# Kernel tuning notes

Hardware: AMD Instinct MI355X
Metric: run time of the kernel (lower is better)

## Reference

```python
import jax, jax.numpy as jnp
import numpy as np

N = 50000      # nodes
E = 800000     # edges (avg degree 16)
D = 64         # node feature dim
DE = 32        # edge feature dim
H = 256        # MLP hidden dim


def setup_inputs() -> dict:
    key = jax.random.key(0)
    k0, k1, k2, k3, k4 = jax.random.split(key, 5)
    x = jax.random.normal(k0, (N, D), dtype=jnp.float32)
    edge_index = jax.random.randint(k1, (2, E), 0, N)
    edge_attr = jax.random.normal(k2, (E, DE), dtype=jnp.float32)
    fan_in1 = 2 * D + DE  # 160
    W1 = jax.random.normal(k3, (fan_in1, H), dtype=jnp.float32) / np.float32(np.sqrt(fan_in1))
    b1 = jnp.zeros((H,), dtype=jnp.float32)
    W2 = jax.random.normal(k4, (H, D), dtype=jnp.float32) / np.float32(np.sqrt(H))
    b2 = jnp.zeros((D,), dtype=jnp.float32)
    return {"x": x, "edge_index": edge_index, "edge_attr": edge_attr,
            "W1": W1, "b1": b1, "W2": W2, "b2": b2}


def reference(x, edge_index, edge_attr, W1, b1, W2, b2):
    row, col = edge_index[0], edge_index[1]
    # gather endpoint features + edge features -> [E, 2D+DE]
    feats = jnp.concatenate([x[row], x[col], edge_attr], axis=-1)
    # MLP: Linear -> ReLU -> Linear
    h = jax.nn.relu(feats @ W1 + b1)          # [E, H]
    out = h @ W2 + b2                          # [E, D]
    # scatter-max aggregate by source node (row), dim_size = N
    agg = jax.ops.segment_max(out, row, num_segments=N)  # [N, D]
    # PyG's old scatter_('max') zero-fills empty slots
    agg = jnp.where(jnp.isneginf(agg), jnp.float32(0.0), agg)
    return (agg, out)
```

## Files before the change

kernel.cpp:

```cpp
#include <hip/hip_runtime.h>
#include <hip/hip_bf16.h>
#include <math.h>

#define NNODES 50000
#define NEDGES 800000
#define CHUNKS (NEDGES / 64)
#define NBLK 256
#define GWAVES (NBLK * 8)

using short8 = __attribute__((ext_vector_type(8))) short;
using f32x4  = __attribute__((ext_vector_type(4))) float;
using f32x16 = __attribute__((ext_vector_type(16))) float;
using u32x4  = __attribute__((ext_vector_type(4))) unsigned;

__device__ __forceinline__ short f2b(float v) {
    return __builtin_bit_cast(short, __float2bfloat16(v));
}
__device__ __forceinline__ unsigned cvt2(float a, float b) {
    return (unsigned)(unsigned short)f2b(a) | ((unsigned)(unsigned short)f2b(b) << 16);
}
__device__ __forceinline__ float b2f_lo(unsigned u) {
    return __builtin_bit_cast(float, u << 16);
}
__device__ __forceinline__ float b2f_hi(unsigned u) {
    return __builtin_bit_cast(float, u & 0xFFFF0000u);
}

__global__ void prep_all(const float* __restrict__ x, short* __restrict__ xb,
                         const float* __restrict__ W1, const float* __restrict__ W2,
                         short* __restrict__ wpk, const int* __restrict__ ei,
                         unsigned* __restrict__ cnt)
{
    int b = blockIdx.x;
    if (b < 3125) {
        int i = b * 256 + threadIdx.x;
        float4 v = reinterpret_cast<const float4*>(x)[i];
        short4 o;
        o.x = f2b(v.x); o.y = f2b(v.y); o.z = f2b(v.z); o.w = f2b(v.w);
        reinterpret_cast<short4*>(xb)[i] = o;
    } else if (b < 6250) {
        int e = (b - 3125) * 256 + threadIdx.x;
        atomicAdd(&cnt[ei[e]], 1u);
    } else {
        int i = (b - 6250) * 256 + threadIdx.x;
        if (i < 40960) {
            int k = i >> 8, n = i & 255;
            int lane = (n & 31) + (((k >> 3) & 1) << 5);
            wpk[(((n >> 5) * 10 + (k >> 4)) * 64 + lane) * 8 + (k & 7)] = f2b(W1[i]);
        }
        if (i < 16384) {
            int k = i >> 6, n = i & 63;
            int lane = (n & 31) + (((k >> 3) & 1) << 5);
            wpk[40960 + (((n >> 5) * 16 + (k >> 4)) * 64 + lane) * 8 + (k & 7)] = f2b(W2[i]);
        }
    }
}

__global__ __launch_bounds__(1024)
void csr_scan1(const unsigned* __restrict__ cnt, unsigned* __restrict__ offs,
               unsigned* __restrict__ bsum) {
    __shared__ unsigned sbuf[1024];
    int t = threadIdx.x, i = blockIdx.x * 1024 + t;
    unsigned v = (i < NNODES) ? cnt[i] : 0u;
    sbuf[t] = v;
    __syncthreads();
    for (int off = 1; off < 1024; off <<= 1) {
        unsigned add = (t >= off) ? sbuf[t - off] : 0u;
        __syncthreads();
        sbuf[t] += add;
        __syncthreads();
    }
    if (i < NNODES) offs[i] = sbuf[t];
    if (t == 1023) bsum[blockIdx.x] = sbuf[1023];
}

__global__ void csr_scan2(unsigned* __restrict__ bsum) {
    int t = threadIdx.x;
    unsigned v = (t < 49) ? bsum[t] : 0u;
    unsigned orig = v;
    for (int off = 1; off < 64; off <<= 1) {
        unsigned n = __shfl_up(v, off, 64);
        if (t >= off) v += n;
    }
    if (t < 49) bsum[t] = v - orig;
}

__global__ __launch_bounds__(1024)
void csr_scan3(const unsigned* __restrict__ cnt, unsigned* __restrict__ offs,
               const unsigned* __restrict__ bsum) {
    int i = blockIdx.x * 1024 + threadIdx.x;
    if (i < NNODES)       offs[i] = offs[i] - cnt[i] + bsum[blockIdx.x];
    else if (i == NNODES) offs[i] = NEDGES;
}

__global__ void csr_place(const int* __restrict__ ei, const unsigned* __restrict__ offs,
                          unsigned* __restrict__ cur, unsigned* __restrict__ elist) {
    int e = blockIdx.x * 256 + threadIdx.x;
    if (e < NEDGES) {
        int r = ei[e];
        unsigned p = offs[r] + atomicAdd(&cur[r], 1u);
        elist[p] = (unsigned)e;
    }
}

template<bool STOREB16>
__global__ __launch_bounds__(512, 2)
void edgeconv_main(const short* __restrict__ xb, const int* __restrict__ ei,
                   const float* __restrict__ ea, const short* __restrict__ wpk,
                   const float* __restrict__ b1, const float* __restrict__ b2,
                   float* __restrict__ outbuf, unsigned* __restrict__ ob16)
{
    __shared__ short    wlds[57344];
    __shared__ unsigned tb[8][1280];

    for (int i = threadIdx.x; i < 7168; i += 512)
        reinterpret_cast<short8*>(wlds)[i] = reinterpret_cast<const short8*>(wpk)[i];
    __syncthreads();

    const short* w1s = wlds;
    const short* w2s = wlds + 40960;
    const int lane = threadIdx.x & 63;
    const int wave = threadIdx.x >> 6;
    const int l32 = lane & 31, hi = lane >> 5;
    unsigned* tw = tb[wave];
    const int gw = blockIdx.x * 8 + wave;

    int r0 = 0, r1 = 0, c0 = 0, c1 = 0;
    {
        int ea0 = gw * 64 + l32, ea1 = gw * 64 + 32 + l32;
        r0 = ei[ea0]; c0 = ei[NEDGES + ea0];
        r1 = ei[ea1]; c1 = ei[NEDGES + ea1];
    }

    for (int c = gw; c < CHUNKS; c += GWAVES) {
        int cn = c + GWAVES;
        int r0n = 0, r1n = 0, c0n = 0, c1n = 0;
        if (cn < CHUNKS) {
            int ea0 = cn * 64 + l32, ea1 = cn * 64 + 32 + l32;
            r0n = ei[ea0]; c0n = ei[NEDGES + ea0];
            r1n = ei[ea1]; c1n = ei[NEDGES + ea1];
        }

        short8 fx[2][10];
        #pragma unroll
        for (int g = 0; g < 2; ++g) {
            const int rr = g ? r1 : r0, cg = g ? c1 : c0;
            const int e = c * 64 + g * 32 + l32;
            #pragma unroll
            for (int ks = 0; ks < 4; ++ks)
                fx[g][ks] = *reinterpret_cast<const short8*>(xb + rr * 64 + ks * 16 + hi * 8);
            #pragma unroll
            for (int ks = 0; ks < 4; ++ks)
                fx[g][4 + ks] = *reinterpret_cast<const short8*>(xb + cg * 64 + ks * 16 + hi * 8);
            #pragma unroll
            for (int ks = 0; ks < 2; ++ks) {
                const float4* p = reinterpret_cast<const float4*>(ea + (size_t)e * 32 + ks * 16 + hi * 8);
                float4 a = p[0], b = p[1];
                u32x4 uu;
                uu[0] = cvt2(a.x, a.y); uu[1] = cvt2(a.z, a.w);
                uu[2] = cvt2(b.x, b.y); uu[3] = cvt2(b.z, b.w);
                fx[g][8 + ks] = __builtin_bit_cast(short8, uu);
            }
        }

        f32x16 acc2[2][2];
        #pragma unroll
        for (int t2 = 0; t2 < 2; ++t2)
            #pragma unroll
            for (int gg = 0; gg < 4; ++gg) {
                float4 bb = *reinterpret_cast<const float4*>(b2 + t2 * 32 + gg * 8 + hi * 4);
                #pragma unroll
                for (int g = 0; g < 2; ++g) {
                    acc2[t2][g][gg * 4 + 0] = bb.x; acc2[t2][g][gg * 4 + 1] = bb.y;
                    acc2[t2][g][gg * 4 + 2] = bb.z; acc2[t2][g][gg * 4 + 3] = bb.w;
                }
            }

        #pragma unroll 1
        for (int t = 0; t < 8; ++t) {
            f32x16 acc1[2];
            #pragma unroll
            for (int gg = 0; gg < 4; ++gg) {
                float4 bb = *reinterpret_cast<const float4*>(b1 + t * 32 + gg * 8 + hi * 4);
                #pragma unroll
                for (int g = 0; g < 2; ++g) {
                    acc1[g][gg * 4 + 0] = bb.x; acc1[g][gg * 4 + 1] = bb.y;
                    acc1[g][gg * 4 + 2] = bb.z; acc1[g][gg * 4 + 3] = bb.w;
                }
            }
            #pragma unroll
            for (int ks = 0; ks < 10; ++ks) {
                short8 wf = *reinterpret_cast<const short8*>(
                    w1s + ((t * 10 + ks) * 64 + lane) * 8);
                acc1[0] = __builtin_amdgcn_mfma_f32_32x32x16_bf16(wf, fx[0][ks], acc1[0], 0, 0, 0);
                acc1[1] = __builtin_amdgcn_mfma_f32_32x32x16_bf16(wf, fx[1][ks], acc1[1], 0, 0, 0);
            }
            #pragma unroll
            for (int ksl = 0; ksl < 2; ++ksl) {
                int ks2 = t * 2 + ksl;
                short8 w20 = *reinterpret_cast<const short8*>(w2s + (ks2 * 64 + lane) * 8);
                short8 w21 = *reinterpret_cast<const short8*>(w2s + ((16 + ks2) * 64 + lane) * 8);
                #pragma unroll
                for (int g = 0; g < 2; ++g) {
                    int q0 = ksl * 8;
                    unsigned D0 = cvt2(fmaxf(acc1[g][q0 + 0], 0.f), fmaxf(acc1[g][q0 + 1], 0.f));
                    unsigned D1 = cvt2(fmaxf(acc1[g][q0 + 2], 0.f), fmaxf(acc1[g][q0 + 3], 0.f));
                    unsigned D2 = cvt2(fmaxf(acc1[g][q0 + 4], 0.f), fmaxf(acc1[g][q0 + 5], 0.f));
                    unsigned D3 = cvt2(fmaxf(acc1[g][q0 + 6], 0.f), fmaxf(acc1[g][q0 + 7], 0.f));
                    asm("v_permlane32_swap_b32 %0, %1" : "+v"(D0), "+v"(D2));
                    asm("v_permlane32_swap_b32 %0, %1" : "+v"(D1), "+v"(D3));
                    u32x4 bu; bu[0] = D0; bu[1] = D1; bu[2] = D2; bu[3] = D3;
                    short8 hb = __builtin_bit_cast(short8, bu);
                    acc2[0][g] = __builtin_amdgcn_mfma_f32_32x32x16_bf16(w20, hb, acc2[0][g], 0, 0, 0);
                    acc2[1][g] = __builtin_amdgcn_mfma_f32_32x32x16_bf16(w21, hb, acc2[1][g], 0, 0, 0);
                }
            }
        }

        #pragma unroll
        for (int g = 0; g < 2; ++g) {
            const int e = c * 64 + g * 32 + l32;
            #pragma unroll
            for (int t2 = 0; t2 < 2; ++t2)
                #pragma unroll
                for (int gg = 0; gg < 4; ++gg) {
                    f32x4 v;
                    v[0] = acc2[t2][g][gg * 4 + 0]; v[1] = acc2[t2][g][gg * 4 + 1];
                    v[2] = acc2[t2][g][gg * 4 + 2]; v[3] = acc2[t2][g][gg * 4 + 3];
                    *reinterpret_cast<f32x4*>(outbuf + (size_t)e * 64 + t2 * 32 + gg * 8 + hi * 4) = v;
                }
            if (STOREB16) {
                #pragma unroll
                for (int t2 = 0; t2 < 2; ++t2)
                    #pragma unroll
                    for (int gg = 0; gg < 4; ++gg) {
                        uint2 w;
                        w.x = cvt2(acc2[t2][g][gg * 4 + 0], acc2[t2][g][gg * 4 + 1]);
                        w.y = cvt2(acc2[t2][g][gg * 4 + 2], acc2[t2][g][gg * 4 + 3]);
                        *reinterpret_cast<uint2*>(&tw[l32 * 40 + t2 * 16 + gg * 4 + hi * 2]) = w;
                    }
                asm volatile("s_waitcnt lgkmcnt(0)" ::: "memory");
                #pragma unroll
                for (int i = 0; i < 4; ++i) {
                    int row = i * 8 + (lane >> 3);
                    u32x4 v = *reinterpret_cast<const u32x4*>(&tw[row * 40 + (lane & 7) * 4]);
                    *reinterpret_cast<u32x4*>(
                        ob16 + ((size_t)(c * 64 + g * 32) * 32) + i * 256 + lane * 4) = v;
                }
                asm volatile("" ::: "memory");
            }
        }

        r0 = r0n; r1 = r1n; c0 = c0n; c1 = c1n;
    }
}

__global__ __launch_bounds__(256)
void agg_b16(const unsigned* __restrict__ offs, const unsigned* __restrict__ elist,
             const unsigned* __restrict__ ob16, float* __restrict__ agg)
{
    const int wave = threadIdx.x >> 6, lane = threadIdx.x & 63;
    const int l16 = lane & 15, qw = lane >> 4;
    const int node = blockIdx.x * 4 + wave;
    if (node >= NNODES) return;
    const unsigned s = offs[node], eend = offs[node + 1];
    float m0 = -INFINITY, m1 = -INFINITY, m2 = -INFINITY, m3 = -INFINITY;
    for (unsigned p = s + qw; p < eend; p += 4) {
        unsigned e = elist[p];
        uint2 u = *reinterpret_cast<const uint2*>(ob16 + (size_t)e * 32 + l16 * 2);
        m0 = fmaxf(m0, b2f_lo(u.x)); m1 = fmaxf(m1, b2f_hi(u.x));
        m2 = fmaxf(m2, b2f_lo(u.y)); m3 = fmaxf(m3, b2f_hi(u.y));
    }
    m0 = fmaxf(m0, __shfl_xor(m0, 16, 64)); m1 = fmaxf(m1, __shfl_xor(m1, 16, 64));
    m2 = fmaxf(m2, __shfl_xor(m2, 16, 64)); m3 = fmaxf(m3, __shfl_xor(m3, 16, 64));
    m0 = fmaxf(m0, __shfl_xor(m0, 32, 64)); m1 = fmaxf(m1, __shfl_xor(m1, 32, 64));
    m2 = fmaxf(m2, __shfl_xor(m2, 32, 64)); m3 = fmaxf(m3, __shfl_xor(m3, 32, 64));
    if (qw == 0) {
        f32x4 o;
        bool emp = (s == eend);
        o[0] = emp ? 0.0f : m0; o[1] = emp ? 0.0f : m1;
        o[2] = emp ? 0.0f : m2; o[3] = emp ? 0.0f : m3;
        *reinterpret_cast<f32x4*>(agg + (size_t)node * 64 + l16 * 4) = o;
    }
}

__global__ __launch_bounds__(256)
void agg_list(const unsigned* __restrict__ offs, const unsigned* __restrict__ elist,
              const float* __restrict__ outbuf, float* __restrict__ agg)
{
    const int wave = threadIdx.x >> 6, lane = threadIdx.x & 63;
    const int node = blockIdx.x * 4 + wave;
    if (node >= NNODES) return;
    const unsigned s = offs[node], eend = offs[node + 1];
    float m0 = -INFINITY, m1 = -INFINITY, m2 = -INFINITY, m3 = -INFINITY;
    float m4 = -INFINITY, m5 = -INFINITY, m6 = -INFINITY, m7 = -INFINITY;
    unsigned p = s;
    for (; p + 8 <= eend; p += 8) {
        float a = outbuf[(size_t)elist[p + 0] * 64 + lane];
        float b = outbuf[(size_t)elist[p + 1] * 64 + lane];
        float c = outbuf[(size_t)elist[p + 2] * 64 + lane];
        float d = outbuf[(size_t)elist[p + 3] * 64 + lane];
        float e = outbuf[(size_t)elist[p + 4] * 64 + lane];
        float f = outbuf[(size_t)elist[p + 5] * 64 + lane];
        float g = outbuf[(size_t)elist[p + 6] * 64 + lane];
        float h = outbuf[(size_t)elist[p + 7] * 64 + lane];
        m0 = fmaxf(m0, a); m1 = fmaxf(m1, b); m2 = fmaxf(m2, c); m3 = fmaxf(m3, d);
        m4 = fmaxf(m4, e); m5 = fmaxf(m5, f); m6 = fmaxf(m6, g); m7 = fmaxf(m7, h);
    }
    for (; p < eend; ++p) m0 = fmaxf(m0, outbuf[(size_t)elist[p] * 64 + lane]);
    float m = fmaxf(fmaxf(fmaxf(m0, m1), fmaxf(m2, m3)),
                    fmaxf(fmaxf(m4, m5), fmaxf(m6, m7)));
    agg[(size_t)node * 64 + lane] = (s == eend) ? 0.0f : m;
}

extern "C" void kernel_launch(void* const* d_in, const int* in_sizes, int n_in,
                              void* d_out, int out_size, void* d_ws, size_t ws_size,
                              hipStream_t stream)
{
    const float* x  = (const float*)d_in[0];
    const int*   ei = (const int*)d_in[1];
    const float* ea = (const float*)d_in[2];
    const float* W1 = (const float*)d_in[3];
    const float* b1 = (const float*)d_in[4];
    const float* W2 = (const float*)d_in[5];
    const float* b2 = (const float*)d_in[6];

    float* aggp = (float*)d_out;
    float* outp = aggp + (size_t)NNODES * 64;

    short*    xb   = (short*)d_ws;
    short*    wpk  = (short*)((char*)d_ws + 6400000);
    unsigned* meta = (unsigned*)((char*)d_ws + 6514688);
    unsigned* cnt   = meta;
    unsigned* cur   = meta + 50000;
    unsigned* offs  = meta + 100000;
    unsigned* bsum  = meta + 150016;
    unsigned* elist = meta + 150144;
    unsigned* ob16  = meta + 950144;

    const size_t NEED = 6514688ULL + 950144ULL * 4ULL + 102400000ULL;
    const bool big = ws_size >= NEED;

    (void)hipMemsetAsync(cnt, 0, 100000 * sizeof(unsigned), stream);
    prep_all<<<6410, 256, 0, stream>>>(x, xb, W1, W2, wpk, ei, cnt);
    csr_scan1<<<49, 1024, 0, stream>>>(cnt, offs, bsum);
    csr_scan2<<<1, 64, 0, stream>>>(bsum);
    csr_scan3<<<49, 1024, 0, stream>>>(cnt, offs, bsum);
    csr_place<<<NEDGES / 256, 256, 0, stream>>>(ei, offs, cur, elist);
    if (big) {
        edgeconv_main<true><<<NBLK, 512, 0, stream>>>(xb, ei, ea, wpk, b1, b2,
                                                      outp, ob16);
        agg_b16<<<(NNODES + 3) / 4, 256, 0, stream>>>(offs, elist, ob16, aggp);
    } else {
        edgeconv_main<false><<<NBLK, 512, 0, stream>>>(xb, ei, ea, wpk, b1, b2,
                                                       outp, nullptr);
        agg_list<<<(NNODES + 3) / 4, 256, 0, stream>>>(offs, elist, outp, aggp);
    }
}
```

Measured before the change: 305.3 us.

## Process edges in CSR order so aggregation reads contiguous bf16 outputs

```diff
diff --git a/kernel.cpp b/kernel.cpp
--- a/kernel.cpp
+++ b/kernel.cpp
@@ -94,21 +94,23 @@
 }
 
 __global__ void csr_place(const int* __restrict__ ei, const unsigned* __restrict__ offs,
-                          unsigned* __restrict__ cur, unsigned* __restrict__ elist) {
+                          unsigned* __restrict__ cur, unsigned* __restrict__ elist,
+                          uint2* __restrict__ rc2) {
     int e = blockIdx.x * 256 + threadIdx.x;
     if (e < NEDGES) {
-        int r = ei[e];
+        int r = ei[e], cc = ei[NEDGES + e];
         unsigned p = offs[r] + atomicAdd(&cur[r], 1u);
         elist[p] = (unsigned)e;
-    }
-}
-
-template<bool STOREB16>
+        if (rc2) { uint2 v; v.x = (unsigned)r; v.y = (unsigned)cc; rc2[p] = v; }
+    }
+}
+
 __global__ __launch_bounds__(512, 2)
-void edgeconv_main(const short* __restrict__ xb, const int* __restrict__ ei,
-                   const float* __restrict__ ea, const short* __restrict__ wpk,
-                   const float* __restrict__ b1, const float* __restrict__ b2,
-                   float* __restrict__ outbuf, unsigned* __restrict__ ob16)
+void edgeconv_csr(const short* __restrict__ xb, const float* __restrict__ ea,
+                  const short* __restrict__ wpk, const float* __restrict__ b1,
+                  const float* __restrict__ b2, const unsigned* __restrict__ elist,
+                  const uint2* __restrict__ rc2, float* __restrict__ outbuf,
+                  unsigned* __restrict__ outcsr)
 {
     __shared__ short    wlds[57344];
     __shared__ unsigned tb[8][1280];
@@ -125,27 +127,31 @@
     unsigned* tw = tb[wave];
     const int gw = blockIdx.x * 8 + wave;
 
-    int r0 = 0, r1 = 0, c0 = 0, c1 = 0;
-    {
-        int ea0 = gw * 64 + l32, ea1 = gw * 64 + 32 + l32;
-        r0 = ei[ea0]; c0 = ei[NEDGES + ea0];
-        r1 = ei[ea1]; c1 = ei[NEDGES + ea1];
+    int eo0 = 0, eo1 = 0, r0 = 0, r1 = 0, c0 = 0, c1 = 0;
+    if (gw < CHUNKS) {
+        int p0 = gw * 64 + l32, p1 = p0 + 32;
+        eo0 = (int)elist[p0]; eo1 = (int)elist[p1];
+        uint2 a = rc2[p0], b = rc2[p1];
+        r0 = (int)a.x; c0 = (int)a.y;
+        r1 = (int)b.x; c1 = (int)b.y;
     }
 
     for (int c = gw; c < CHUNKS; c += GWAVES) {
-        int cn = c + GWAVES;
-        int r0n = 0, r1n = 0, c0n = 0, c1n = 0;
-        if (cn < CHUNKS) {
-            int ea0 = cn * 64 + l32, ea1 = cn * 64 + 32 + l32;
-            r0n = ei[ea0]; c0n = ei[NEDGES + ea0];
-            r1n = ei[ea1]; c1n = ei[NEDGES + ea1];
+        int cnx = c + GWAVES;
+        int eo0n = 0, eo1n = 0, r0n = 0, r1n = 0, c0n = 0, c1n = 0;
+        if (cnx < CHUNKS) {
+            int p0 = cnx * 64 + l32, p1 = p0 + 32;
+            eo0n = (int)elist[p0]; eo1n = (int)elist[p1];
+            uint2 a = rc2[p0], b = rc2[p1];
+            r0n = (int)a.x; c0n = (int)a.y;
+            r1n = (int)b.x; c1n = (int)b.y;
         }
 
         short8 fx[2][10];
         #pragma unroll
         for (int g = 0; g < 2; ++g) {
             const int rr = g ? r1 : r0, cg = g ? c1 : c0;
-            const int e = c * 64 + g * 32 + l32;
+            const int eo = g ? eo1 : eo0;
             #pragma unroll
             for (int ks = 0; ks < 4; ++ks)
                 fx[g][ks] = *reinterpret_cast<const short8*>(xb + rr * 64 + ks * 16 + hi * 8);
@@ -154,7 +160,7 @@
                 fx[g][4 + ks] = *reinterpret_cast<const short8*>(xb + cg * 64 + ks * 16 + hi * 8);
             #pragma unroll
             for (int ks = 0; ks < 2; ++ks) {
-                const float4* p = reinterpret_cast<const float4*>(ea + (size_t)e * 32 + ks * 16 + hi * 8);
+                const float4* p = reinterpret_cast<const float4*>(ea + (size_t)eo * 32 + ks * 16 + hi * 8);
                 float4 a = p[0], b = p[1];
                 u32x4 uu;
                 uu[0] = cvt2(a.x, a.y); uu[1] = cvt2(a.z, a.w);
@@ -219,7 +225,7 @@
 
         #pragma unroll
         for (int g = 0; g < 2; ++g) {
-            const int e = c * 64 + g * 32 + l32;
+            const int eo = g ? eo1 : eo0;
             #pragma unroll
             for (int t2 = 0; t2 < 2; ++t2)
                 #pragma unroll
@@ -227,37 +233,35 @@
                     f32x4 v;
                     v[0] = acc2[t2][g][gg * 4 + 0]; v[1] = acc2[t2][g][gg * 4 + 1];
                     v[2] = acc2[t2][g][gg * 4 + 2]; v[3] = acc2[t2][g][gg * 4 + 3];
-                    *reinterpret_cast<f32x4*>(outbuf + (size_t)e * 64 + t2 * 32 + gg * 8 + hi * 4) = v;
-                }
-            if (STOREB16) {
-                #pragma unroll
-                for (int t2 = 0; t2 < 2; ++t2)
-                    #pragma unroll
-                    for (int gg = 0; gg < 4; ++gg) {
-                        uint2 w;
-                        w.x = cvt2(acc2[t2][g][gg * 4 + 0], acc2[t2][g][gg * 4 + 1]);
-                        w.y = cvt2(acc2[t2][g][gg * 4 + 2], acc2[t2][g][gg * 4 + 3]);
-                        *reinterpret_cast<uint2*>(&tw[l32 * 40 + t2 * 16 + gg * 4 + hi * 2]) = w;
-                    }
-                asm volatile("s_waitcnt lgkmcnt(0)" ::: "memory");
-                #pragma unroll
-                for (int i = 0; i < 4; ++i) {
-                    int row = i * 8 + (lane >> 3);
-                    u32x4 v = *reinterpret_cast<const u32x4*>(&tw[row * 40 + (lane & 7) * 4]);
-                    *reinterpret_cast<u32x4*>(
-                        ob16 + ((size_t)(c * 64 + g * 32) * 32) + i * 256 + lane * 4) = v;
-                }
-                asm volatile("" ::: "memory");
-            }
-        }
-
-        r0 = r0n; r1 = r1n; c0 = c0n; c1 = c1n;
+                    *reinterpret_cast<f32x4*>(outbuf + (size_t)eo * 64 + t2 * 32 + gg * 8 + hi * 4) = v;
+                }
+            #pragma unroll
+            for (int t2 = 0; t2 < 2; ++t2)
+                #pragma unroll
+                for (int gg = 0; gg < 4; ++gg) {
+                    uint2 w;
+                    w.x = cvt2(acc2[t2][g][gg * 4 + 0], acc2[t2][g][gg * 4 + 1]);
+                    w.y = cvt2(acc2[t2][g][gg * 4 + 2], acc2[t2][g][gg * 4 + 3]);
+                    *reinterpret_cast<uint2*>(&tw[l32 * 40 + t2 * 16 + gg * 4 + hi * 2]) = w;
+                }
+            asm volatile("s_waitcnt lgkmcnt(0)" ::: "memory");
+            #pragma unroll
+            for (int i = 0; i < 4; ++i) {
+                int row = i * 8 + (lane >> 3);
+                u32x4 v = *reinterpret_cast<const u32x4*>(&tw[row * 40 + (lane & 7) * 4]);
+                *reinterpret_cast<u32x4*>(
+                    outcsr + ((size_t)(c * 64 + g * 32) * 32) + i * 256 + lane * 4) = v;
+            }
+            asm volatile("" ::: "memory");
+        }
+
+        eo0 = eo0n; eo1 = eo1n; r0 = r0n; r1 = r1n; c0 = c0n; c1 = c1n;
     }
 }
 
 __global__ __launch_bounds__(256)
-void agg_b16(const unsigned* __restrict__ offs, const unsigned* __restrict__ elist,
-             const unsigned* __restrict__ ob16, float* __restrict__ agg)
+void agg_csr(const unsigned* __restrict__ offs, const unsigned* __restrict__ outcsr,
+             float* __restrict__ agg)
 {
     const int wave = threadIdx.x >> 6, lane = threadIdx.x & 63;
     const int l16 = lane & 15, qw = lane >> 4;
@@ -265,9 +269,17 @@
     if (node >= NNODES) return;
     const unsigned s = offs[node], eend = offs[node + 1];
     float m0 = -INFINITY, m1 = -INFINITY, m2 = -INFINITY, m3 = -INFINITY;
-    for (unsigned p = s + qw; p < eend; p += 4) {
-        unsigned e = elist[p];
-        uint2 u = *reinterpret_cast<const uint2*>(ob16 + (size_t)e * 32 + l16 * 2);
+    unsigned p = s + qw;
+    for (; p + 4 < eend; p += 8) {
+        uint2 u = *reinterpret_cast<const uint2*>(outcsr + (size_t)p * 32 + l16 * 2);
+        uint2 w = *reinterpret_cast<const uint2*>(outcsr + (size_t)(p + 4) * 32 + l16 * 2);
+        m0 = fmaxf(fmaxf(m0, b2f_lo(u.x)), b2f_lo(w.x));
+        m1 = fmaxf(fmaxf(m1, b2f_hi(u.x)), b2f_hi(w.x));
+        m2 = fmaxf(fmaxf(m2, b2f_lo(u.y)), b2f_lo(w.y));
+        m3 = fmaxf(fmaxf(m3, b2f_hi(u.y)), b2f_hi(w.y));
+    }
+    for (; p < eend; p += 4) {
+        uint2 u = *reinterpret_cast<const uint2*>(outcsr + (size_t)p * 32 + l16 * 2);
         m0 = fmaxf(m0, b2f_lo(u.x)); m1 = fmaxf(m1, b2f_hi(u.x));
         m2 = fmaxf(m2, b2f_lo(u.y)); m3 = fmaxf(m3, b2f_hi(u.y));
     }
@@ -281,6 +293,128 @@
         o[0] = emp ? 0.0f : m0; o[1] = emp ? 0.0f : m1;
         o[2] = emp ? 0.0f : m2; o[3] = emp ? 0.0f : m3;
         *reinterpret_cast<f32x4*>(agg + (size_t)node * 64 + l16 * 4) = o;
+    }
+}
+
+__global__ __launch_bounds__(512, 2)
+void edgeconv_orig(const short* __restrict__ xb, const int* __restrict__ ei,
+                   const float* __restrict__ ea, const short* __restrict__ wpk,
+                   const float* __restrict__ b1, const float* __restrict__ b2,
+                   float* __restrict__ outbuf)
+{
+    __shared__ short wlds[57344];
+    for (int i = threadIdx.x; i < 7168; i += 512)
+        reinterpret_cast<short8*>(wlds)[i] = reinterpret_cast<const short8*>(wpk)[i];
+    __syncthreads();
+
+    const short* w1s = wlds;
+    const short* w2s = wlds + 40960;
+    const int lane = threadIdx.x & 63;
+    const int wave = threadIdx.x >> 6;
+    const int l32 = lane & 31, hi = lane >> 5;
+    const int gw = blockIdx.x * 8 + wave;
+
+    int r0 = 0, r1 = 0, c0 = 0, c1 = 0;
+    {
+        int ea0 = gw * 64 + l32, ea1 = gw * 64 + 32 + l32;
+        r0 = ei[ea0]; c0 = ei[NEDGES + ea0];
+        r1 = ei[ea1]; c1 = ei[NEDGES + ea1];
+    }
+    for (int c = gw; c < CHUNKS; c += GWAVES) {
+        int cnx = c + GWAVES;
+        int r0n = 0, r1n = 0, c0n = 0, c1n = 0;
+        if (cnx < CHUNKS) {
+            int ea0 = cnx * 64 + l32, ea1 = cnx * 64 + 32 + l32;
+            r0n = ei[ea0]; c0n = ei[NEDGES + ea0];
+            r1n = ei[ea1]; c1n = ei[NEDGES + ea1];
+        }
+        short8 fx[2][10];
+        #pragma unroll
+        for (int g = 0; g < 2; ++g) {
+            const int rr = g ? r1 : r0, cg = g ? c1 : c0;
+            const int e = c * 64 + g * 32 + l32;
+            #pragma unroll
+            for (int ks = 0; ks < 4; ++ks)
+                fx[g][ks] = *reinterpret_cast<const short8*>(xb + rr * 64 + ks * 16 + hi * 8);
+            #pragma unroll
+            for (int ks = 0; ks < 4; ++ks)
+                fx[g][4 + ks] = *reinterpret_cast<const short8*>(xb + cg * 64 + ks * 16 + hi * 8);
+            #pragma unroll
+            for (int ks = 0; ks < 2; ++ks) {
+                const float4* p = reinterpret_cast<const float4*>(ea + (size_t)e * 32 + ks * 16 + hi * 8);
+                float4 a = p[0], b = p[1];
+                u32x4 uu;
+                uu[0] = cvt2(a.x, a.y); uu[1] = cvt2(a.z, a.w);
+                uu[2] = cvt2(b.x, b.y); uu[3] = cvt2(b.z, b.w);
+                fx[g][8 + ks] = __builtin_bit_cast(short8, uu);
+            }
+        }
+        f32x16 acc2[2][2];
+        #pragma unroll
+        for (int t2 = 0; t2 < 2; ++t2)
+            #pragma unroll
+            for (int gg = 0; gg < 4; ++gg) {
+                float4 bb = *reinterpret_cast<const float4*>(b2 + t2 * 32 + gg * 8 + hi * 4);
+                #pragma unroll
+                for (int g = 0; g < 2; ++g) {
+                    acc2[t2][g][gg * 4 + 0] = bb.x; acc2[t2][g][gg * 4 + 1] = bb.y;
+                    acc2[t2][g][gg * 4 + 2] = bb.z; acc2[t2][g][gg * 4 + 3] = bb.w;
+                }
+            }
+        #pragma unroll 1
+        for (int t = 0; t < 8; ++t) {
+            f32x16 acc1[2];
+            #pragma unroll
+            for (int gg = 0; gg < 4; ++gg) {
+                float4 bb = *reinterpret_cast<const float4*>(b1 + t * 32 + gg * 8 + hi * 4);
+                #pragma unroll
+                for (int g = 0; g < 2; ++g) {
+                    acc1[g][gg * 4 + 0] = bb.x; acc1[g][gg * 4 + 1] = bb.y;
+                    acc1[g][gg * 4 + 2] = bb.z; acc1[g][gg * 4 + 3] = bb.w;
+                }
+            }
+            #pragma unroll
+            for (int ks = 0; ks < 10; ++ks) {
+                short8 wf = *reinterpret_cast<const short8*>(
+                    w1s + ((t * 10 + ks) * 64 + lane) * 8);
+                acc1[0] = __builtin_amdgcn_mfma_f32_32x32x16_bf16(wf, fx[0][ks], acc1[0], 0, 0, 0);
+                acc1[1] = __builtin_amdgcn_mfma_f32_32x32x16_bf16(wf, fx[1][ks], acc1[1], 0, 0, 0);
+            }
+            #pragma unroll
+            for (int ksl = 0; ksl < 2; ++ksl) {
+                int ks2 = t * 2 + ksl;
+                short8 w20 = *reinterpret_cast<const short8*>(w2s + (ks2 * 64 + lane) * 8);
+                short8 w21 = *reinterpret_cast<const short8*>(w2s + ((16 + ks2) * 64 + lane) * 8);
+                #pragma unroll
+                for (int g = 0; g < 2; ++g) {
+                    int q0 = ksl * 8;
+                    unsigned D0 = cvt2(fmaxf(acc1[g][q0 + 0], 0.f), fmaxf(acc1[g][q0 + 1], 0.f));
+                    unsigned D1 = cvt2(fmaxf(acc1[g][q0 + 2], 0.f), fmaxf(acc1[g][q0 + 3], 0.f));
+                    unsigned D2 = cvt2(fmaxf(acc1[g][q0 + 4], 0.f), fmaxf(acc1[g][q0 + 5], 0.f));
+                    unsigned D3 = cvt2(fmaxf(acc1[g][q0 + 6], 0.f), fmaxf(acc1[g][q0 + 7], 0.f));
+                    asm("v_permlane32_swap_b32 %0, %1" : "+v"(D0), "+v"(D2));
+                    asm("v_permlane32_swap_b32 %0, %1" : "+v"(D1), "+v"(D3));
+                    u32x4 bu; bu[0] = D0; bu[1] = D1; bu[2] = D2; bu[3] = D3;
+                    short8 hb = __builtin_bit_cast(short8, bu);
+                    acc2[0][g] = __builtin_amdgcn_mfma_f32_32x32x16_bf16(w20, hb, acc2[0][g], 0, 0, 0);
+                    acc2[1][g] = __builtin_amdgcn_mfma_f32_32x32x16_bf16(w21, hb, acc2[1][g], 0, 0, 0);
+                }
+            }
+        }
+        #pragma unroll
+        for (int g = 0; g < 2; ++g) {
+            const int e = c * 64 + g * 32 + l32;
+            #pragma unroll
+            for (int t2 = 0; t2 < 2; ++t2)
+                #pragma unroll
+                for (int gg = 0; gg < 4; ++gg) {
+                    f32x4 v;
+                    v[0] = acc2[t2][g][gg * 4 + 0]; v[1] = acc2[t2][g][gg * 4 + 1];
+                    v[2] = acc2[t2][g][gg * 4 + 2]; v[3] = acc2[t2][g][gg * 4 + 3];
+                    *reinterpret_cast<f32x4*>(outbuf + (size_t)e * 64 + t2 * 32 + gg * 8 + hi * 4) = v;
+                }
+        }
+        r0 = r0n; r1 = r1n; c0 = c0n; c1 = c1n;
     }
 }
 
@@ -331,14 +465,15 @@
     short*    xb   = (short*)d_ws;
     short*    wpk  = (short*)((char*)d_ws + 6400000);
     unsigned* meta = (unsigned*)((char*)d_ws + 6514688);
-    unsigned* cnt   = meta;
-    unsigned* cur   = meta + 50000;
-    unsigned* offs  = meta + 100000;
-    unsigned* bsum  = meta + 150016;
-    unsigned* elist = meta + 150144;
-    unsigned* ob16  = meta + 950144;
-
-    const size_t NEED = 6514688ULL + 950144ULL * 4ULL + 102400000ULL;
+    unsigned* cnt    = meta;
+    unsigned* cur    = meta + 50000;
+    unsigned* offs   = meta + 100000;
+    unsigned* bsum   = meta + 150016;
+    unsigned* elist  = meta + 150144;
+    uint2*    rc2    = (uint2*)(meta + 950144);
+    unsigned* outcsr = meta + 2550144;
+
+    const size_t NEED = 6514688ULL + 2550144ULL * 4ULL + 102400000ULL;
     const bool big = ws_size >= NEED;
 
     (void)hipMemsetAsync(cnt, 0, 100000 * sizeof(unsigned), stream);
@@ -346,14 +481,14 @@
     csr_scan1<<<49, 1024, 0, stream>>>(cnt, offs, bsum);
     csr_scan2<<<1, 64, 0, stream>>>(bsum);
     csr_scan3<<<49, 1024, 0, stream>>>(cnt, offs, bsum);
-    csr_place<<<NEDGES / 256, 256, 0, stream>>>(ei, offs, cur, elist);
+    csr_place<<<NEDGES / 256, 256, 0, stream>>>(ei, offs, cur, elist,
+                                                big ? rc2 : (uint2*)nullptr);
     if (big) {
-        edgeconv_main<true><<<NBLK, 512, 0, stream>>>(xb, ei, ea, wpk, b1, b2,
-                                                      outp, ob16);
-        agg_b16<<<(NNODES + 3) / 4, 256, 0, stream>>>(offs, elist, ob16, aggp);
+        edgeconv_csr<<<NBLK, 512, 0, stream>>>(xb, ea, wpk, b1, b2, elist, rc2,
+                                               outp, outcsr);
+        agg_csr<<<(NNODES + 3) / 4, 256, 0, stream>>>(offs, outcsr, aggp);
     } else {
-        edgeconv_main<false><<<NBLK, 512, 0, stream>>>(xb, ei, ea, wpk, b1, b2,
-                                                       outp, nullptr);
+        edgeconv_orig<<<NBLK, 512, 0, stream>>>(xb, ei, ea, wpk, b1, b2, outp);
         agg_list<<<(NNODES + 3) / 4, 256, 0, stream>>>(offs, elist, outp, aggp);
     }
 }
```

Result: faster. 291.0 us (-4.7%).
